# Optimization experiments

Hardware: AMD Instinct MI355X
Metric: run time of the kernel (lower is better)

Reference implementation:

```python
import jax, jax.numpy as jnp
import numpy as np

B, T, L, INPUT_DIM = 16, 128, 100, 100
EMB = 100
FEAT = INPUT_DIM + 3 * EMB          # 400
HID, OUT = 128, 50
RNN_IN = 2 * INPUT_DIM + 3 * L      # 500
VOCAB = 10000 + 2


def setup_inputs() -> dict:
    key = jax.random.key(0)
    ks = jax.random.split(key, 12)
    first = jax.random.normal(ks[0], (B, T, INPUT_DIM), jnp.float32)
    idx = jax.random.randint(ks[1], (B, T, 3 * L), 0, VOCAB).astype(jnp.float32)
    x = jnp.concatenate([first, idx], axis=2)  # [B,T,400]
    s = 0.05
    return {
        "x": x,
        "embed_nodes": jax.random.normal(ks[2], (VOCAB, EMB), jnp.float32) * s,
        "embed_paths": jax.random.normal(ks[3], (VOCAB, EMB), jnp.float32) * s,
        "W_t": jax.random.normal(ks[4], (FEAT, FEAT), jnp.float32) / np.sqrt(FEAT),
        "b_t": jnp.zeros((FEAT,), jnp.float32),
        "W_a": jax.random.normal(ks[5], (FEAT, 1), jnp.float32) / np.sqrt(FEAT),
        "b_a": jnp.zeros((1,), jnp.float32),
        "W_ih": jax.random.normal(ks[6], (4 * HID, RNN_IN), jnp.float32) / np.sqrt(RNN_IN),
        "W_hh": jax.random.normal(ks[7], (4 * HID, HID), jnp.float32) / np.sqrt(HID),
        "b_ih": jnp.zeros((4 * HID,), jnp.float32),
        "b_hh": jnp.zeros((4 * HID,), jnp.float32),
        "W_fc": jax.random.normal(ks[8], (HID, OUT), jnp.float32) / np.sqrt(HID),
        "b_fc": jnp.zeros((OUT,), jnp.float32),
    }


def _lstm(xs, W_ih, W_hh, b_ih, b_hh):
    # xs: [B,T,D] -> out [B,T,H]; PyTorch gate order i,f,g,o
    def step(carry, xt):
        h, c = carry
        g = xt @ W_ih.T + h @ W_hh.T + (b_ih + b_hh)  # [B,4H]
        i, f, gg, o = jnp.split(g, 4, axis=-1)
        c = jax.nn.sigmoid(f) * c + jax.nn.sigmoid(i) * jnp.tanh(gg)
        h = jax.nn.sigmoid(o) * jnp.tanh(c)
        return (h, c), h
    h0 = jnp.zeros((xs.shape[0], HID), xs.dtype)
    (_, _), hs = jax.lax.scan(step, (h0, h0), jnp.swapaxes(xs, 0, 1))
    return jnp.swapaxes(hs, 0, 1)


def reference(x, embed_nodes, embed_paths, W_t, b_t, W_a, b_a,
              W_ih, W_hh, b_ih, b_hh, W_fc, b_fc):
    first = x[:, :, :INPUT_DIM]                                   # [B,T,100]
    c2v = x[:, :, INPUT_DIM:INPUT_DIM + 3 * L].reshape(B, T, L, 3).astype(jnp.int32)
    s_emb = embed_nodes[c2v[..., 0]]                              # [B,T,L,100]
    e_emb = embed_nodes[c2v[..., 2]]
    p_emb = embed_paths[c2v[..., 1]]
    att_part = jnp.broadcast_to(first[:, :, None, :], (B, T, L, INPUT_DIM))
    full = jnp.concatenate([s_emb, e_emb, p_emb, att_part], axis=3)  # [B,T,L,400]
    # dropout skipped (deterministic reference == evaluating=True path)
    transformed = jnp.tanh(full @ W_t + b_t)
    ctx = transformed @ W_a + b_a                                 # [B,T,L,1]
    # faithful to nn.Softmax(dim=1): softmax over the sequence axis T
    attn = jax.nn.softmax(ctx, axis=1)
    code_vectors = jnp.sum(full * attn, axis=2)                   # [B,T,400]
    rnn_input = jnp.concatenate([first, code_vectors], axis=2)    # [B,T,500]
    out = _lstm(rnn_input, W_ih, W_hh, b_ih, b_hh)                # [B,T,128]
    return jax.nn.sigmoid(out @ W_fc + b_fc)                      # [B,T,50]
```

## Files before the change

kernel.cpp:

```cpp
#include <hip/hip_runtime.h>
#include <hip/hip_bf16.h>
#include <stdint.h>

#define B_     16
#define T_     128
#define L_     100
#define IN_    100
#define EMB_   100
#define FEAT_  400
#define HID_   128
#define OUT_   50
#define RNNIN_ 500
#define VOCAB_ 10002
#define BT_    2048

#if defined(__has_builtin)
#if __has_builtin(__builtin_amdgcn_cvt_pk_f32_fp8) && __has_builtin(__builtin_amdgcn_cvt_pk_fp8_f32)
#define HAVE_FP8 1
#endif
#endif
#ifndef HAVE_FP8
#define HAVE_FP8 0
#endif

typedef __attribute__((ext_vector_type(8))) short short8;
typedef __attribute__((ext_vector_type(4))) float f32x4;
typedef __attribute__((ext_vector_type(2))) float v2f;

__device__ __forceinline__ float lo2f(unsigned int u) {
    union { unsigned int i; float f; } v; v.i = u << 16; return v.f;
}
__device__ __forceinline__ float hi2f(unsigned int u) {
    union { unsigned int i; float f; } v; v.i = u & 0xffff0000u; return v.f;
}
__device__ __forceinline__ float fast_tanh(float x) {
    x = fminf(15.f, fmaxf(-15.f, x));
    float e = __expf(2.f * x);
    return (e - 1.f) * __builtin_amdgcn_rcpf(e + 1.f);
}
__device__ __forceinline__ float sigm(float x) {
    x = fminf(30.f, fmaxf(-30.f, x));
    float e = __expf(-x);
    return __builtin_amdgcn_rcpf(1.f + e);
}

__device__ __forceinline__ void table_gemm_body(
    const float* __restrict__ A, int lda, int rows,
    const float* __restrict__ Wt, int wrow,
    const float* __restrict__ bias, void* __restrict__ outp, int mode, int r0)
{
    __shared__ float As[32][100];
    int tid = threadIdx.x;
    for (int i = tid; i < 3200; i += 256) {
        int r = i / 100, c = i - r * 100;
        int gr = r0 + r;
        As[r][c] = (gr < rows) ? A[(size_t)gr * lda + c] : 0.f;
    }
    __syncthreads();
    int jj = tid & 63, rr = tid >> 6;
    float acc[8][7];
#pragma unroll
    for (int k = 0; k < 8; k++)
#pragma unroll
        for (int m = 0; m < 7; m++) acc[k][m] = 0.f;
    for (int i = 0; i < 100; i++) {
        float w[7];
#pragma unroll
        for (int m = 0; m < 7; m++) {
            int j = jj + (m << 6);
            w[m] = (j < 400) ? Wt[(size_t)(wrow + i) * 400 + j] : 0.f;
        }
#pragma unroll
        for (int k = 0; k < 8; k++) {
            float a = As[rr * 8 + k][i];
#pragma unroll
            for (int m = 0; m < 7; m++) acc[k][m] = fmaf(a, w[m], acc[k][m]);
        }
    }
#pragma unroll
    for (int k = 0; k < 8; k++) {
        int gr = r0 + rr * 8 + k;
        if (gr >= rows) continue;
#pragma unroll
        for (int m = 0; m < 7; m++) {
            int j = jj + (m << 6);
            if (j >= 400) continue;
            float v = acc[k][m];
            if (bias) v += bias[j];
#if HAVE_FP8
            if (mode == 2) {
                unsigned u = (unsigned)__builtin_amdgcn_cvt_pk_fp8_f32(v, v, 0, false);
                ((unsigned char*)outp)[(size_t)gr * 400 + j] = (unsigned char)(u & 0xff);
            } else
#endif
            if (mode == 1) ((__hip_bfloat16*)outp)[(size_t)gr * 400 + j] = __float2bfloat16(v);
            else           ((float*)outp)[(size_t)gr * 400 + j] = v;
        }
    }
}

#if HAVE_FP8
#define TBL_MODE 2
#else
#define TBL_MODE 1
#endif

#define EGRID 313

__global__ __launch_bounds__(256) void setup_k(
    const float* __restrict__ x, const float* __restrict__ EN,
    const float* __restrict__ EP, const float* __restrict__ Wt,
    const float* __restrict__ bt, const float* __restrict__ Wih,
    const float* __restrict__ Whh,
    float* __restrict__ q,
    void* __restrict__ Es, void* __restrict__ Ee, void* __restrict__ Epb,
    __hip_bfloat16* __restrict__ ENb, __hip_bfloat16* __restrict__ EPb,
    float* __restrict__ WihT, __hip_bfloat16* __restrict__ Whh_bf)
{
    int blk = blockIdx.x;
    if (blk < 64) {
        table_gemm_body(x, 400, BT_, Wt, 300, bt, (void*)q, 0, blk * 32);
    } else if (blk < 64 + 3 * EGRID) {
        int t = blk - 64;
        int which = t / EGRID, r0 = (t - which * EGRID) * 32;
        const float* A = (which == 2) ? EP : EN;
        void* o = (which == 0) ? Es : ((which == 1) ? Ee : Epb);
        table_gemm_body(A, 100, VOCAB_, Wt, which * 100, nullptr, o, TBL_MODE, r0);
    } else {
        int t0 = (blk - (64 + 3 * EGRID)) * 256 + threadIdx.x;
        const int stride = 256 * 256;
        int n1 = VOCAB_ * 100;
        for (int i = t0; i < n1; i += stride) ENb[i] = __float2bfloat16(EN[i]);
        for (int i = t0; i < n1; i += stride) EPb[i] = __float2bfloat16(EP[i]);
        for (int i = t0; i < 512 * 500; i += stride) {
            int r = i / 500, c = i - r * 500;
            WihT[(size_t)c * 512 + r] = Wih[i];
        }
        for (int i = t0; i < 512 * 128; i += stride) Whh_bf[i] = __float2bfloat16(Whh[i]);
    }
}

__global__ __launch_bounds__(256) void stage_a(
    const float* __restrict__ x,
    const void* __restrict__ Esv, const void* __restrict__ Eev,
    const void* __restrict__ Epv,
    const float* __restrict__ q, const float* __restrict__ Wa,
    float* __restrict__ ctx)
{
    __shared__ int idx_s[300];
    int bt = blockIdx.x, tid = threadIdx.x;
    const float* xr = x + (size_t)bt * 400 + 100;
    for (int i = tid; i < 300; i += 256) idx_s[i] = (int)xr[i];
    int lane = tid & 63, wave = tid >> 6;
    bool act = lane < 50;
    int j0 = lane * 8;
    float qv[8], wv[8];
    if (act) {
        float4 qa = *(const float4*)(q + (size_t)bt * 400 + j0);
        float4 qb = *(const float4*)(q + (size_t)bt * 400 + j0 + 4);
        float4 wa = *(const float4*)(Wa + j0);
        float4 wb = *(const float4*)(Wa + j0 + 4);
        qv[0]=qa.x; qv[1]=qa.y; qv[2]=qa.z; qv[3]=qa.w;
        qv[4]=qb.x; qv[5]=qb.y; qv[6]=qb.z; qv[7]=qb.w;
        wv[0]=wa.x; wv[1]=wa.y; wv[2]=wa.z; wv[3]=wa.w;
        wv[4]=wb.x; wv[5]=wb.y; wv[6]=wb.z; wv[7]=wb.w;
    } else {
#pragma unroll
        for (int jj = 0; jj < 8; jj++) { qv[jj] = 0.f; wv[jj] = 0.f; }
    }
    __syncthreads();
    for (int l = wave; l < 100; l += 4) {
        int i0 = idx_s[3 * l], i1 = idx_s[3 * l + 1], i2 = idx_s[3 * l + 2];
        float sum = 0.f;
        if (act) {
            float zs[8];
#if HAVE_FP8
            const unsigned char* Es8 = (const unsigned char*)Esv;
            const unsigned char* Ee8 = (const unsigned char*)Eev;
            const unsigned char* Ep8 = (const unsigned char*)Epv;
            uint2 a  = ((const uint2*)(Es8 + (size_t)i0 * 400))[lane];
            uint2 b  = ((const uint2*)(Ee8 + (size_t)i2 * 400))[lane];
            uint2 cc = ((const uint2*)(Ep8 + (size_t)i1 * 400))[lane];
            v2f s01 = __builtin_amdgcn_cvt_pk_f32_fp8((int)a.x, false);
            v2f s23 = __builtin_amdgcn_cvt_pk_f32_fp8((int)a.x, true);
            v2f s45 = __builtin_amdgcn_cvt_pk_f32_fp8((int)a.y, false);
            v2f s67 = __builtin_amdgcn_cvt_pk_f32_fp8((int)a.y, true);
            v2f e01 = __builtin_amdgcn_cvt_pk_f32_fp8((int)b.x, false);
            v2f e23 = __builtin_amdgcn_cvt_pk_f32_fp8((int)b.x, true);
            v2f e45 = __builtin_amdgcn_cvt_pk_f32_fp8((int)b.y, false);
            v2f e67 = __builtin_amdgcn_cvt_pk_f32_fp8((int)b.y, true);
            v2f p01 = __builtin_amdgcn_cvt_pk_f32_fp8((int)cc.x, false);
            v2f p23 = __builtin_amdgcn_cvt_pk_f32_fp8((int)cc.x, true);
            v2f p45 = __builtin_amdgcn_cvt_pk_f32_fp8((int)cc.y, false);
            v2f p67 = __builtin_amdgcn_cvt_pk_f32_fp8((int)cc.y, true);
            zs[0] = s01.x + e01.x + p01.x + qv[0];
            zs[1] = s01.y + e01.y + p01.y + qv[1];
            zs[2] = s23.x + e23.x + p23.x + qv[2];
            zs[3] = s23.y + e23.y + p23.y + qv[3];
            zs[4] = s45.x + e45.x + p45.x + qv[4];
            zs[5] = s45.y + e45.y + p45.y + qv[5];
            zs[6] = s67.x + e67.x + p67.x + qv[6];
            zs[7] = s67.y + e67.y + p67.y + qv[7];
#else
            const __hip_bfloat16* Es = (const __hip_bfloat16*)Esv;
            const __hip_bfloat16* Ee = (const __hip_bfloat16*)Eev;
            const __hip_bfloat16* Ep = (const __hip_bfloat16*)Epv;
            uint4 a  = *((const uint4*)(Es + (size_t)i0 * 400) + lane);
            uint4 b  = *((const uint4*)(Ee + (size_t)i2 * 400) + lane);
            uint4 cc = *((const uint4*)(Ep + (size_t)i1 * 400) + lane);
            zs[0] = lo2f(a.x)+lo2f(b.x)+lo2f(cc.x)+qv[0];
            zs[1] = hi2f(a.x)+hi2f(b.x)+hi2f(cc.x)+qv[1];
            zs[2] = lo2f(a.y)+lo2f(b.y)+lo2f(cc.y)+qv[2];
            zs[3] = hi2f(a.y)+hi2f(b.y)+hi2f(cc.y)+qv[3];
            zs[4] = lo2f(a.z)+lo2f(b.z)+lo2f(cc.z)+qv[4];
            zs[5] = hi2f(a.z)+hi2f(b.z)+hi2f(cc.z)+qv[5];
            zs[6] = lo2f(a.w)+lo2f(b.w)+lo2f(cc.w)+qv[6];
            zs[7] = hi2f(a.w)+hi2f(b.w)+hi2f(cc.w)+qv[7];
#endif
#pragma unroll
            for (int jj = 0; jj < 8; jj++) sum = fmaf(fast_tanh(zs[jj]), wv[jj], sum);
        }
#pragma unroll
        for (int off = 32; off; off >>= 1) sum += __shfl_xor(sum, off);
        if (lane == 0) ctx[(size_t)bt * 100 + l] = sum;
    }
}

__global__ __launch_bounds__(256) void softmax_w(
    const float* __restrict__ ctx, float* __restrict__ attn)
{
    int wid = blockIdx.x * 4 + (threadIdx.x >> 6);
    int lane = threadIdx.x & 63;
    int b = wid / 100, l = wid - b * 100;
    size_t base = (size_t)b * 128 * 100 + l;
    float v0 = ctx[base + (size_t)lane * 100];
    float v1 = ctx[base + (size_t)(lane + 64) * 100];
    float m = fmaxf(v0, v1);
#pragma unroll
    for (int off = 32; off; off >>= 1) m = fmaxf(m, __shfl_xor(m, off));
    float e0 = __expf(v0 - m), e1 = __expf(v1 - m);
    float s = e0 + e1;
#pragma unroll
    for (int off = 32; off; off >>= 1) s += __shfl_xor(s, off);
    float rs = 1.f / s;
    attn[base + (size_t)lane * 100] = e0 * rs;
    attn[base + (size_t)(lane + 64) * 100] = e1 * rs;
}

__global__ __launch_bounds__(128) void stage_c(
    const float* __restrict__ x, const float* __restrict__ attn,
    const unsigned short* __restrict__ ENb, const unsigned short* __restrict__ EPb,
    float* __restrict__ cv)
{
    __shared__ float at[100];
    __shared__ int idx[300];
    int bt = blockIdx.x, tid = threadIdx.x;
    if (tid < 100) at[tid] = attn[(size_t)bt * 100 + tid];
    const float* xr = x + (size_t)bt * 400 + 100;
    for (int i = tid; i < 300; i += 128) idx[i] = (int)xr[i];
    __syncthreads();
    int d = tid;
    if (d < 100) {
        float as = 0.f, ae = 0.f, ap = 0.f, sa = 0.f;
#pragma unroll 4
        for (int l = 0; l < 100; l++) {
            float a = at[l]; sa += a;
            as = fmaf(a, lo2f(ENb[(size_t)idx[3 * l] * 100 + d]), as);
            ae = fmaf(a, lo2f(ENb[(size_t)idx[3 * l + 2] * 100 + d]), ae);
            ap = fmaf(a, lo2f(EPb[(size_t)idx[3 * l + 1] * 100 + d]), ap);
        }
        float* o = cv + (size_t)bt * 400;
        o[d] = as; o[100 + d] = ae; o[200 + d] = ap;
        o[300 + d] = x[(size_t)bt * 400 + d] * sa;
    }
}

__global__ __launch_bounds__(512) void gemm_x(
    const float* __restrict__ x, const float* __restrict__ cv,
    const float* __restrict__ WihT, const float* __restrict__ bih,
    const float* __restrict__ bhh, float* __restrict__ X)
{
    __shared__ float ins[8][500];
    int r0 = blockIdx.x * 8, tid = threadIdx.x;
    for (int i = tid; i < 4000; i += 512) {
        int r = i / 500, k = i - r * 500;
        ins[r][k] = (k < 100) ? x[(size_t)(r0 + r) * 400 + k]
                              : cv[(size_t)(r0 + r) * 400 + (k - 100)];
    }
    __syncthreads();
    int g = tid;
    float acc[8];
#pragma unroll
    for (int r = 0; r < 8; r++) acc[r] = 0.f;
    for (int k4 = 0; k4 < 125; k4++) {
        int k = k4 * 4;
        float w0 = WihT[(size_t)k * 512 + g];
        float w1 = WihT[(size_t)(k + 1) * 512 + g];
        float w2 = WihT[(size_t)(k + 2) * 512 + g];
        float w3 = WihT[(size_t)(k + 3) * 512 + g];
#pragma unroll
        for (int r = 0; r < 8; r++) {
            float4 a = *(const float4*)&ins[r][k];
            acc[r] = fmaf(a.x, w0, fmaf(a.y, w1, fmaf(a.z, w2, fmaf(a.w, w3, acc[r]))));
        }
    }
    float bias = bih[g] + bhh[g];
#pragma unroll
    for (int r = 0; r < 8; r++) X[(size_t)(r0 + r) * 512 + g] = acc[r] + bias;
}

__global__ __launch_bounds__(512, 1) void lstm_k(
    const float* __restrict__ X, const __hip_bfloat16* __restrict__ Whh_bf,
    float* __restrict__ hs)
{
    int b = blockIdx.x, tid = threadIdx.x;
    int wave = tid >> 6, lane = tid & 63;
    int col = lane & 15, kg = lane >> 4;

    short8 bf[4][4];
#pragma unroll
    for (int n = 0; n < 4; n++) {
        int g = n * 128 + wave * 16 + col;
#pragma unroll
        for (int kk = 0; kk < 4; kk++)
            bf[n][kk] = *(const short8*)(Whh_bf + (size_t)g * 128 + kk * 32 + kg * 8);
    }

    __shared__ __hip_bfloat16 hbuf[2][128];
    __shared__ float Xs[16][512];
    __shared__ float hsb_s[16][128];
    float c = 0.f;
    if (tid < 128) hbuf[0][tid] = __float2bfloat16(0.f);
    const float* xb = X + (size_t)b * 128 * 512;
    float* hb = hs + (size_t)b * 128 * 128;
    int j = wave * 16 + col;
    int p = 0;

    __syncthreads();

    for (int tc = 0; tc < 8; tc++) {
        {
            const float* src = xb + (size_t)tc * 16 * 512 + tid;
#pragma unroll
            for (int k = 0; k < 16; k++) Xs[k][tid] = src[k * 512];
        }
        __syncthreads();

#pragma unroll 1
        for (int ts = 0; ts < 16; ts++) {
            short8 af[4];
            short8 zz = {};
#pragma unroll
            for (int kk = 0; kk < 4; kk++) {
                af[kk] = zz;
                if (col == 0) af[kk] = *(const short8*)(&hbuf[p][0] + kk * 32 + kg * 8);
            }
            f32x4 acc[4];
#pragma unroll
            for (int n = 0; n < 4; n++) acc[n] = (f32x4){0.f, 0.f, 0.f, 0.f};
#pragma unroll
            for (int kk = 0; kk < 4; kk++)
#pragma unroll
                for (int n = 0; n < 4; n++)
                    acc[n] = __builtin_amdgcn_mfma_f32_16x16x32_bf16(af[kk], bf[n][kk], acc[n], 0, 0, 0);

            if (lane < 16) {
                float pi = acc[0][0] + Xs[ts][j];
                float pf = acc[1][0] + Xs[ts][128 + j];
                float pg = acc[2][0] + Xs[ts][256 + j];
                float po = acc[3][0] + Xs[ts][384 + j];
                c = sigm(pf) * c + sigm(pi) * fast_tanh(pg);
                float hn = sigm(po) * fast_tanh(c);
                hbuf[p ^ 1][j] = __float2bfloat16(hn);
                hsb_s[ts][j] = hn;
            }
            __syncthreads();
            p ^= 1;
        }

        {
            float* dst = hb + (size_t)tc * 16 * 128;
#pragma unroll
            for (int k = 0; k < 4; k++) {
                int i = k * 512 + tid;
                dst[i] = hsb_s[i >> 7][i & 127];
            }
        }
    }
}

__global__ __launch_bounds__(64) void fc_k(
    const float* __restrict__ hs, const float* __restrict__ Wfc,
    const float* __restrict__ bfc, float* __restrict__ out)
{
    int r0 = blockIdx.x * 4, o = threadIdx.x;
    if (o >= 50) return;
    float acc[4] = {0.f, 0.f, 0.f, 0.f};
    for (int j = 0; j < 128; j++) {
        float wv = Wfc[j * 50 + o];
#pragma unroll
        for (int r = 0; r < 4; r++)
            acc[r] = fmaf(hs[(size_t)(r0 + r) * 128 + j], wv, acc[r]);
    }
    float bb = bfc[o];
#pragma unroll
    for (int r = 0; r < 4; r++) out[(size_t)(r0 + r) * 50 + o] = sigm(acc[r] + bb);
}

extern "C" void kernel_launch(void* const* d_in, const int* in_sizes, int n_in,
                              void* d_out, int out_size, void* d_ws, size_t ws_size,
                              hipStream_t stream) {
    const float* x   = (const float*)d_in[0];
    const float* EN  = (const float*)d_in[1];
    const float* EP  = (const float*)d_in[2];
    const float* Wt  = (const float*)d_in[3];
    const float* bt  = (const float*)d_in[4];
    const float* Wa  = (const float*)d_in[5];
    const float* Wih = (const float*)d_in[7];
    const float* Whh = (const float*)d_in[8];
    const float* bih = (const float*)d_in[9];
    const float* bhh = (const float*)d_in[10];
    const float* Wfc = (const float*)d_in[11];
    const float* bfc = (const float*)d_in[12];
    float* out = (float*)d_out;

    char* ws = (char*)d_ws;
    size_t off = 0;
    auto alloc = [&](size_t bytes) -> char* {
        char* p = ws + off;
        off = (off + bytes + 255) & ~(size_t)255;
        return p;
    };
    void* Es  = (void*)alloc((size_t)VOCAB_ * 400 * 2);
    void* Ee  = (void*)alloc((size_t)VOCAB_ * 400 * 2);
    void* Epb = (void*)alloc((size_t)VOCAB_ * 400 * 2);
    __hip_bfloat16* ENb = (__hip_bfloat16*)alloc((size_t)VOCAB_ * 100 * 2);
    __hip_bfloat16* EPb = (__hip_bfloat16*)alloc((size_t)VOCAB_ * 100 * 2);
    float* q    = (float*)alloc((size_t)BT_ * 400 * 4);
    float* ctx  = (float*)alloc((size_t)BT_ * 100 * 4);
    float* attn = (float*)alloc((size_t)BT_ * 100 * 4);
    float* cv   = (float*)alloc((size_t)BT_ * 400 * 4);
    float* X    = (float*)alloc((size_t)BT_ * 512 * 4);
    float* hsb  = (float*)alloc((size_t)BT_ * 128 * 4);
    float* WihT = (float*)alloc((size_t)500 * 512 * 4);
    __hip_bfloat16* Whh_bf = (__hip_bfloat16*)alloc((size_t)512 * 128 * 2);

    setup_k<<<64 + 3 * EGRID + 256, 256, 0, stream>>>(
        x, EN, EP, Wt, bt, Wih, Whh,
        q, Es, Ee, Epb, ENb, EPb, WihT, Whh_bf);

    stage_a<<<BT_, 256, 0, stream>>>(x, Es, Ee, Epb, q, Wa, ctx);
    softmax_w<<<400, 256, 0, stream>>>(ctx, attn);
    stage_c<<<BT_, 128, 0, stream>>>(x, attn, (const unsigned short*)ENb,
                                     (const unsigned short*)EPb, cv);
    gemm_x<<<BT_ / 8, 512, 0, stream>>>(x, cv, WihT, bih, bhh, X);
    lstm_k<<<B_, 512, 0, stream>>>(X, Whh_bf, hsb);
    fc_k<<<BT_ / 4, 64, 0, stream>>>(hsb, Wfc, bfc, out);
}
```

Measured before the change: 266.7 us.

## Move table projections and input gate GEMM onto bf16 MFMA

Replaces the scalar fp32 table-projection GEMMs (embedding tables times W_t slices, and x times W_t) with bf16 MFMA 16x16x32 kernels that read pre-cast bf16 inputs and a transposed, zero-padded W_t. The setup is split into a cast kernel followed by a matmul kernel. The LSTM input-projection GEMM also moves to MFMA: stage_c now writes a padded bf16 rnn input row directly. This targets the FMA-bound setup and gemm_x work, at the cost of an extra launch, bf16 rounding of the GEMM inputs, and a serial dependency between the cast and matmul kernels.

```diff
diff --git a/kernel.cpp b/kernel.cpp
--- a/kernel.cpp
+++ b/kernel.cpp
@@ -13,6 +13,7 @@
 #define RNNIN_ 500
 #define VOCAB_ 10002
 #define BT_    2048
+#define TBLK   157
 
 #if defined(__has_builtin)
 #if __has_builtin(__builtin_amdgcn_cvt_pk_f32_fp8) && __has_builtin(__builtin_amdgcn_cvt_pk_fp8_f32)
@@ -24,6 +25,7 @@
 #endif
 
 typedef __attribute__((ext_vector_type(8))) short short8;
+typedef __attribute__((ext_vector_type(4))) short short4v;
 typedef __attribute__((ext_vector_type(4))) float f32x4;
 typedef __attribute__((ext_vector_type(2))) float v2f;
 
@@ -44,99 +46,112 @@
     return __builtin_amdgcn_rcpf(1.f + e);
 }
 
-__device__ __forceinline__ void table_gemm_body(
-    const float* __restrict__ A, int lda, int rows,
-    const float* __restrict__ Wt, int wrow,
-    const float* __restrict__ bias, void* __restrict__ outp, int mode, int r0)
-{
-    __shared__ float As[32][100];
-    int tid = threadIdx.x;
-    for (int i = tid; i < 3200; i += 256) {
-        int r = i / 100, c = i - r * 100;
-        int gr = r0 + r;
-        As[r][c] = (gr < rows) ? A[(size_t)gr * lda + c] : 0.f;
-    }
-    __syncthreads();
-    int jj = tid & 63, rr = tid >> 6;
-    float acc[8][7];
-#pragma unroll
-    for (int k = 0; k < 8; k++)
-#pragma unroll
-        for (int m = 0; m < 7; m++) acc[k][m] = 0.f;
-    for (int i = 0; i < 100; i++) {
-        float w[7];
-#pragma unroll
-        for (int m = 0; m < 7; m++) {
-            int j = jj + (m << 6);
-            w[m] = (j < 400) ? Wt[(size_t)(wrow + i) * 400 + j] : 0.f;
-        }
-#pragma unroll
-        for (int k = 0; k < 8; k++) {
-            float a = As[rr * 8 + k][i];
-#pragma unroll
-            for (int m = 0; m < 7; m++) acc[k][m] = fmaf(a, w[m], acc[k][m]);
-        }
-    }
-#pragma unroll
-    for (int k = 0; k < 8; k++) {
-        int gr = r0 + rr * 8 + k;
-        if (gr >= rows) continue;
-#pragma unroll
-        for (int m = 0; m < 7; m++) {
-            int j = jj + (m << 6);
-            if (j >= 400) continue;
-            float v = acc[k][m];
-            if (bias) v += bias[j];
+__global__ __launch_bounds__(256) void casts_k(
+    const float* __restrict__ EN, const float* __restrict__ EP,
+    const float* __restrict__ x, const float* __restrict__ Wt,
+    const float* __restrict__ Wih, const float* __restrict__ Whh,
+    __hip_bfloat16* __restrict__ ENb, __hip_bfloat16* __restrict__ EPb,
+    __hip_bfloat16* __restrict__ x_bf, __hip_bfloat16* __restrict__ WtT,
+    __hip_bfloat16* __restrict__ Wih_bf, __hip_bfloat16* __restrict__ Whh_bf)
+{
+    int t0 = blockIdx.x * 256 + threadIdx.x;
+    const int stride = 256 * 256;
+    int n1 = VOCAB_ * 100;
+    for (int i = t0; i < n1; i += stride) ENb[i] = __float2bfloat16(EN[i]);
+    for (int i = t0; i < n1; i += stride) EPb[i] = __float2bfloat16(EP[i]);
+    for (int i = t0; i < BT_ * 100; i += stride) {
+        int bt = i / 100, d = i - bt * 100;
+        x_bf[i] = __float2bfloat16(x[(size_t)bt * 400 + d]);
+    }
+    for (int i = t0; i < 4 * 400 * 128; i += stride) {
+        int w = i / (400 * 128), rem = i - w * 400 * 128;
+        int n = rem >> 7, k = rem & 127;
+        WtT[i] = __float2bfloat16((k < 100) ? Wt[(size_t)(w * 100 + k) * 400 + n] : 0.f);
+    }
+    for (int i = t0; i < 512 * 512; i += stride) {
+        int g = i >> 9, k = i & 511;
+        Wih_bf[i] = __float2bfloat16((k < 500) ? Wih[(size_t)g * 500 + k] : 0.f);
+    }
+    for (int i = t0; i < 512 * 128; i += stride) Whh_bf[i] = __float2bfloat16(Whh[i]);
+}
+
+__device__ __forceinline__ void load_a100(const __hip_bfloat16* __restrict__ arow,
+                                          int kg, short8 af[4])
+{
+    af[0] = *(const short8*)(arow + kg * 8);
+    af[1] = *(const short8*)(arow + 32 + kg * 8);
+    af[2] = *(const short8*)(arow + 64 + kg * 8);
+    short8 z = {};
+    af[3] = z;
+    if (kg == 0) {
+        short4v t = *(const short4v*)(arow + 96);
+        af[3][0] = t[0]; af[3][1] = t[1]; af[3][2] = t[2]; af[3][3] = t[3];
+    }
+}
+
+__global__ __launch_bounds__(256) void mm_k(
+    const __hip_bfloat16* __restrict__ ENb, const __hip_bfloat16* __restrict__ EPb,
+    const __hip_bfloat16* __restrict__ x_bf, const __hip_bfloat16* __restrict__ WtT,
+    const float* __restrict__ btb,
+    void* __restrict__ Es, void* __restrict__ Ee, void* __restrict__ Ep,
+    float* __restrict__ q)
+{
+    int blk = blockIdx.x, tid = threadIdx.x;
+    int wave = tid >> 6, lane = tid & 63;
+    int cl = lane & 15, kg = lane >> 4;
+
+    if (blk < 3 * TBLK) {
+        int which = blk / TBLK, mb = blk - which * TBLK;
+        const __hip_bfloat16* A = (which == 2) ? EPb : ENb;
+        void* outp = (which == 0) ? Es : ((which == 1) ? Ee : Ep);
+        int r0 = mb * 64 + wave * 16;
+        int ra = r0 + cl; if (ra > VOCAB_ - 1) ra = VOCAB_ - 1;
+        short8 af[4];
+        load_a100(A + (size_t)ra * 100, kg, af);
+        const __hip_bfloat16* Bp = WtT + (size_t)which * 400 * 128;
+        for (int n0 = 0; n0 < 25; n0++) {
+            const __hip_bfloat16* brow = Bp + (size_t)(n0 * 16 + cl) * 128 + kg * 8;
+            f32x4 acc = (f32x4){0.f, 0.f, 0.f, 0.f};
+            acc = __builtin_amdgcn_mfma_f32_16x16x32_bf16(af[0], *(const short8*)(brow), acc, 0, 0, 0);
+            acc = __builtin_amdgcn_mfma_f32_16x16x32_bf16(af[1], *(const short8*)(brow + 32), acc, 0, 0, 0);
+            acc = __builtin_amdgcn_mfma_f32_16x16x32_bf16(af[2], *(const short8*)(brow + 64), acc, 0, 0, 0);
+            acc = __builtin_amdgcn_mfma_f32_16x16x32_bf16(af[3], *(const short8*)(brow + 96), acc, 0, 0, 0);
+            int colj = n0 * 16 + cl;
+#pragma unroll
+            for (int r = 0; r < 4; r++) {
+                int gr = r0 + kg * 4 + r;
+                if (gr < VOCAB_) {
+                    float v = acc[r];
 #if HAVE_FP8
-            if (mode == 2) {
-                unsigned u = (unsigned)__builtin_amdgcn_cvt_pk_fp8_f32(v, v, 0, false);
-                ((unsigned char*)outp)[(size_t)gr * 400 + j] = (unsigned char)(u & 0xff);
-            } else
+                    unsigned u = (unsigned)__builtin_amdgcn_cvt_pk_fp8_f32(v, v, 0, false);
+                    ((unsigned char*)outp)[(size_t)gr * 400 + colj] = (unsigned char)(u & 0xff);
+#else
+                    ((__hip_bfloat16*)outp)[(size_t)gr * 400 + colj] = __float2bfloat16(v);
 #endif
-            if (mode == 1) ((__hip_bfloat16*)outp)[(size_t)gr * 400 + j] = __float2bfloat16(v);
-            else           ((float*)outp)[(size_t)gr * 400 + j] = v;
-        }
-    }
-}
-
-#if HAVE_FP8
-#define TBL_MODE 2
-#else
-#define TBL_MODE 1
-#endif
-
-#define EGRID 313
-
-__global__ __launch_bounds__(256) void setup_k(
-    const float* __restrict__ x, const float* __restrict__ EN,
-    const float* __restrict__ EP, const float* __restrict__ Wt,
-    const float* __restrict__ bt, const float* __restrict__ Wih,
-    const float* __restrict__ Whh,
-    float* __restrict__ q,
-    void* __restrict__ Es, void* __restrict__ Ee, void* __restrict__ Epb,
-    __hip_bfloat16* __restrict__ ENb, __hip_bfloat16* __restrict__ EPb,
-    float* __restrict__ WihT, __hip_bfloat16* __restrict__ Whh_bf)
-{
-    int blk = blockIdx.x;
-    if (blk < 64) {
-        table_gemm_body(x, 400, BT_, Wt, 300, bt, (void*)q, 0, blk * 32);
-    } else if (blk < 64 + 3 * EGRID) {
-        int t = blk - 64;
-        int which = t / EGRID, r0 = (t - which * EGRID) * 32;
-        const float* A = (which == 2) ? EP : EN;
-        void* o = (which == 0) ? Es : ((which == 1) ? Ee : Epb);
-        table_gemm_body(A, 100, VOCAB_, Wt, which * 100, nullptr, o, TBL_MODE, r0);
+                }
+            }
+        }
     } else {
-        int t0 = (blk - (64 + 3 * EGRID)) * 256 + threadIdx.x;
-        const int stride = 256 * 256;
-        int n1 = VOCAB_ * 100;
-        for (int i = t0; i < n1; i += stride) ENb[i] = __float2bfloat16(EN[i]);
-        for (int i = t0; i < n1; i += stride) EPb[i] = __float2bfloat16(EP[i]);
-        for (int i = t0; i < 512 * 500; i += stride) {
-            int r = i / 500, c = i - r * 500;
-            WihT[(size_t)c * 512 + r] = Wih[i];
-        }
-        for (int i = t0; i < 512 * 128; i += stride) Whh_bf[i] = __float2bfloat16(Whh[i]);
+        int mb = blk - 3 * TBLK;
+        int r0 = mb * 64 + wave * 16;
+        short8 af[4];
+        load_a100(x_bf + (size_t)(r0 + cl) * 100, kg, af);
+        const __hip_bfloat16* Bp = WtT + (size_t)3 * 400 * 128;
+        for (int n0 = 0; n0 < 25; n0++) {
+            const __hip_bfloat16* brow = Bp + (size_t)(n0 * 16 + cl) * 128 + kg * 8;
+            f32x4 acc = (f32x4){0.f, 0.f, 0.f, 0.f};
+            acc = __builtin_amdgcn_mfma_f32_16x16x32_bf16(af[0], *(const short8*)(brow), acc, 0, 0, 0);
+            acc = __builtin_amdgcn_mfma_f32_16x16x32_bf16(af[1], *(const short8*)(brow + 32), acc, 0, 0, 0);
+            acc = __builtin_amdgcn_mfma_f32_16x16x32_bf16(af[2], *(const short8*)(brow + 64), acc, 0, 0, 0);
+            acc = __builtin_amdgcn_mfma_f32_16x16x32_bf16(af[3], *(const short8*)(brow + 96), acc, 0, 0, 0);
+            int colj = n0 * 16 + cl;
+            float bb = btb[colj];
+#pragma unroll
+            for (int r = 0; r < 4; r++) {
+                int gr = r0 + kg * 4 + r;
+                q[(size_t)gr * 400 + colj] = acc[r] + bb;
+            }
+        }
     }
 }
 
@@ -250,7 +265,7 @@
 __global__ __launch_bounds__(128) void stage_c(
     const float* __restrict__ x, const float* __restrict__ attn,
     const unsigned short* __restrict__ ENb, const unsigned short* __restrict__ EPb,
-    float* __restrict__ cv)
+    __hip_bfloat16* __restrict__ rnn_bf)
 {
     __shared__ float at[100];
     __shared__ int idx[300];
@@ -260,6 +275,7 @@
     for (int i = tid; i < 300; i += 128) idx[i] = (int)xr[i];
     __syncthreads();
     int d = tid;
+    __hip_bfloat16* o = rnn_bf + (size_t)bt * 512;
     if (d < 100) {
         float as = 0.f, ae = 0.f, ap = 0.f, sa = 0.f;
 #pragma unroll 4
@@ -269,44 +285,52 @@
             ae = fmaf(a, lo2f(ENb[(size_t)idx[3 * l + 2] * 100 + d]), ae);
             ap = fmaf(a, lo2f(EPb[(size_t)idx[3 * l + 1] * 100 + d]), ap);
         }
-        float* o = cv + (size_t)bt * 400;
-        o[d] = as; o[100 + d] = ae; o[200 + d] = ap;
-        o[300 + d] = x[(size_t)bt * 400 + d] * sa;
-    }
-}
-
-__global__ __launch_bounds__(512) void gemm_x(
-    const float* __restrict__ x, const float* __restrict__ cv,
-    const float* __restrict__ WihT, const float* __restrict__ bih,
-    const float* __restrict__ bhh, float* __restrict__ X)
-{
-    __shared__ float ins[8][500];
-    int r0 = blockIdx.x * 8, tid = threadIdx.x;
-    for (int i = tid; i < 4000; i += 512) {
-        int r = i / 500, k = i - r * 500;
-        ins[r][k] = (k < 100) ? x[(size_t)(r0 + r) * 400 + k]
-                              : cv[(size_t)(r0 + r) * 400 + (k - 100)];
-    }
-    __syncthreads();
-    int g = tid;
-    float acc[8];
-#pragma unroll
-    for (int r = 0; r < 8; r++) acc[r] = 0.f;
-    for (int k4 = 0; k4 < 125; k4++) {
-        int k = k4 * 4;
-        float w0 = WihT[(size_t)k * 512 + g];
-        float w1 = WihT[(size_t)(k + 1) * 512 + g];
-        float w2 = WihT[(size_t)(k + 2) * 512 + g];
-        float w3 = WihT[(size_t)(k + 3) * 512 + g];
-#pragma unroll
-        for (int r = 0; r < 8; r++) {
-            float4 a = *(const float4*)&ins[r][k];
-            acc[r] = fmaf(a.x, w0, fmaf(a.y, w1, fmaf(a.z, w2, fmaf(a.w, w3, acc[r]))));
-        }
-    }
-    float bias = bih[g] + bhh[g];
-#pragma unroll
-    for (int r = 0; r < 8; r++) X[(size_t)(r0 + r) * 512 + g] = acc[r] + bias;
+        float fi = x[(size_t)bt * 400 + d];
+        o[d]       = __float2bfloat16(fi);
+        o[100 + d] = __float2bfloat16(as);
+        o[200 + d] = __float2bfloat16(ae);
+        o[300 + d] = __float2bfloat16(ap);
+        o[400 + d] = __float2bfloat16(fi * sa);
+    } else if (d < 112) {
+        o[400 + d] = __float2bfloat16(0.f);
+    }
+}
+
+__global__ __launch_bounds__(256) void gemm_x(
+    const __hip_bfloat16* __restrict__ rnn_bf, const __hip_bfloat16* __restrict__ Wih_bf,
+    const float* __restrict__ bih, const float* __restrict__ bhh,
+    float* __restrict__ X)
+{
+    int blk = blockIdx.x, tid = threadIdx.x;
+    int wave = tid >> 6, lane = tid & 63;
+    int cl = lane & 15, kg = lane >> 4;
+    int r0 = blk * 64 + wave * 16;
+
+    short8 af[16];
+    const __hip_bfloat16* arow = rnn_bf + (size_t)(r0 + cl) * 512 + kg * 8;
+#pragma unroll
+    for (int ks = 0; ks < 16; ks++) af[ks] = *(const short8*)(arow + ks * 32);
+
+    for (int n0 = 0; n0 < 32; n0 += 2) {
+        const __hip_bfloat16* b0 = Wih_bf + (size_t)(n0 * 16 + cl) * 512 + kg * 8;
+        const __hip_bfloat16* b1 = b0 + 16 * 512;
+        f32x4 acA = (f32x4){0.f, 0.f, 0.f, 0.f};
+        f32x4 acB = (f32x4){0.f, 0.f, 0.f, 0.f};
+#pragma unroll
+        for (int ks = 0; ks < 16; ks++) {
+            acA = __builtin_amdgcn_mfma_f32_16x16x32_bf16(af[ks], *(const short8*)(b0 + ks * 32), acA, 0, 0, 0);
+            acB = __builtin_amdgcn_mfma_f32_16x16x32_bf16(af[ks], *(const short8*)(b1 + ks * 32), acB, 0, 0, 0);
+        }
+        int c0 = n0 * 16 + cl, c1 = c0 + 16;
+        float bi0 = bih[c0] + bhh[c0];
+        float bi1 = bih[c1] + bhh[c1];
+#pragma unroll
+        for (int r = 0; r < 4; r++) {
+            int m = r0 + kg * 4 + r;
+            X[(size_t)m * 512 + c0] = acA[r] + bi0;
+            X[(size_t)m * 512 + c1] = acB[r] + bi1;
+        }
+    }
 }
 
 __global__ __launch_bounds__(512, 1) void lstm_k(
@@ -434,26 +458,29 @@
     void* Es  = (void*)alloc((size_t)VOCAB_ * 400 * 2);
     void* Ee  = (void*)alloc((size_t)VOCAB_ * 400 * 2);
     void* Epb = (void*)alloc((size_t)VOCAB_ * 400 * 2);
-    __hip_bfloat16* ENb = (__hip_bfloat16*)alloc((size_t)VOCAB_ * 100 * 2);
-    __hip_bfloat16* EPb = (__hip_bfloat16*)alloc((size_t)VOCAB_ * 100 * 2);
+    __hip_bfloat16* ENb    = (__hip_bfloat16*)alloc((size_t)VOCAB_ * 100 * 2);
+    __hip_bfloat16* EPb    = (__hip_bfloat16*)alloc((size_t)VOCAB_ * 100 * 2);
+    __hip_bfloat16* x_bf   = (__hip_bfloat16*)alloc((size_t)BT_ * 100 * 2);
+    __hip_bfloat16* WtT    = (__hip_bfloat16*)alloc((size_t)4 * 400 * 128 * 2);
+    __hip_bfloat16* Wih_bf = (__hip_bfloat16*)alloc((size_t)512 * 512 * 2);
+    __hip_bfloat16* Whh_bf = (__hip_bfloat16*)alloc((size_t)512 * 128 * 2);
+    __hip_bfloat16* rnn_bf = (__hip_bfloat16*)alloc((size_t)BT_ * 512 * 2);
     float* q    = (float*)alloc((size_t)BT_ * 400 * 4);
     float* ctx  = (float*)alloc((size_t)BT_ * 100 * 4);
     float* attn = (float*)alloc((size_t)BT_ * 100 * 4);
-    float* cv   = (float*)alloc((size_t)BT_ * 400 * 4);
     float* X    = (float*)alloc((size_t)BT_ * 512 * 4);
     float* hsb  = (float*)alloc((size_t)BT_ * 128 * 4);
-    float* WihT = (float*)alloc((size_t)500 * 512 * 4);
-    __hip_bfloat16* Whh_bf = (__hip_bfloat16*)alloc((size_t)512 * 128 * 2);
-
-    setup_k<<<64 + 3 * EGRID + 256, 256, 0, stream>>>(
-        x, EN, EP, Wt, bt, Wih, Whh,
-        q, Es, Ee, Epb, ENb, EPb, WihT, Whh_bf);
+
+    casts_k<<<256, 256, 0, stream>>>(EN, EP, x, Wt, Wih, Whh,
+                                     ENb, EPb, x_bf, WtT, Wih_bf, Whh_bf);
+    mm_k<<<3 * TBLK + 32, 256, 0, stream>>>(ENb, EPb, x_bf, WtT, bt,
+                                            Es, Ee, Epb, q);
 
     stage_a<<<BT_, 256, 0, stream>>>(x, Es, Ee, Epb, q, Wa, ctx);
     softmax_w<<<400, 256, 0, stream>>>(ctx, attn);
     stage_c<<<BT_, 128, 0, stream>>>(x, attn, (const unsigned short*)ENb,
-                                     (const unsigned short*)EPb, cv);
-    gemm_x<<<BT_ / 8, 512, 0, stream>>>(x, cv, WihT, bih, bhh, X);
+                                     (const unsigned short*)EPb, rnn_bf);
+    gemm_x<<<32, 256, 0, stream>>>(rnn_bf, Wih_bf, bih, bhh, X);
     lstm_k<<<B_, 512, 0, stream>>>(X, Whh_bf, hsb);
     fc_k<<<BT_ / 4, 64, 0, stream>>>(hsb, Wfc, bfc, out);
 }
```

New measurement: 271.6 us. No clear change (+1.8%).
